# Kernel optimization log

Measured on AMD Instinct MI355X. Metric: run time of the kernel, lower is better.

The kernel has to match this reference:

```python
import jax, jax.numpy as jnp
import numpy as np
import math

DIMS = 2560
N_HEADS = 32
ROT_DIM = 32  # partial rotary (Phi-2)
BASE = 10000.0
B, L = 1, 2048


def apply_rope(x, rot_dim=ROT_DIM, base=BASE, offset=0):
    # x: [B, H, L, hd]; rotate first rot_dim features, pass rest through
    Lx = x.shape[2]
    D = rot_dim // 2
    pos = jnp.arange(offset, offset + Lx, dtype=jnp.float32)              # [L]
    freq = jnp.exp(-jnp.arange(D, dtype=jnp.float32) * (math.log(base) / D))  # [D]
    theta = pos[:, None] * freq[None, :]                                   # [L, D]
    cos, sin = jnp.cos(theta), jnp.sin(theta)
    x1 = x[..., :D]
    x2 = x[..., D:rot_dim]
    rx1 = x1 * cos - x2 * sin
    rx2 = x1 * sin + x2 * cos
    return jnp.concatenate([rx1, rx2, x[..., rot_dim:]], axis=-1)


def setup_inputs() -> dict:
    key = jax.random.key(0)
    k1, k2, k3, k4, k5 = jax.random.split(key, 5)
    x = jax.random.normal(k1, (B, L, DIMS), dtype=jnp.float32)
    Wqkv_w = jax.random.normal(k2, (3 * DIMS, DIMS), dtype=jnp.float32) * 0.02
    Wqkv_b = jax.random.normal(k3, (3 * DIMS,), dtype=jnp.float32) * 0.02
    out_w = jax.random.normal(k4, (DIMS, DIMS), dtype=jnp.float32) * 0.02
    out_b = jax.random.normal(k5, (DIMS,), dtype=jnp.float32) * 0.02
    # additive causal mask, broadcast over batch/heads
    mask = jnp.triu(jnp.full((L, L), -1e9, dtype=jnp.float32), k=1)[None, None]
    return {"x": x, "Wqkv_w": Wqkv_w, "Wqkv_b": Wqkv_b,
            "out_w": out_w, "out_b": out_b, "mask": mask}


def reference(x, Wqkv_w, Wqkv_b, out_w, out_b, mask):
    Bx, Lx, _ = x.shape
    hd = DIMS // N_HEADS  # 80
    qkv = x @ Wqkv_w.T + Wqkv_b                          # [B, L, 3*dims]
    q, k, v = jnp.split(qkv, 3, axis=-1)
    def to_heads(t):
        return t.reshape(Bx, Lx, N_HEADS, hd).transpose(0, 2, 1, 3)  # [B,H,L,hd]
    q, k, v = to_heads(q), to_heads(k), to_heads(v)
    q = apply_rope(q)
    k = apply_rope(k)
    scale = 1.0 / math.sqrt(hd)
    scores = scale * jnp.einsum('bhqd,bhkd->bhqk', q, k) + mask  # [B,H,L,L]
    probs = jax.nn.softmax(scores, axis=-1)
    out = jnp.einsum('bhqk,bhkd->bhqd', probs, v)
    out = out.transpose(0, 2, 1, 3).reshape(Bx, Lx, DIMS)
    return out @ out_w.T + out_b
```

## Files before the change

kernel.cpp:

```cpp
#include <hip/hip_runtime.h>
#include <cstdint>
#include <cmath>

typedef __attribute__((ext_vector_type(4))) float f32x4;
typedef __attribute__((ext_vector_type(8))) short s16x8;

#define LOG2E 1.4426950408889634f

__device__ __forceinline__ unsigned short f2bf(float f) {
    unsigned int u = __float_as_uint(f);
    u += 0x7FFFu + ((u >> 16) & 1u);
    return (unsigned short)(u >> 16);
}
__device__ __forceinline__ float bf2f(unsigned short s) {
    return __uint_as_float(((unsigned int)s) << 16);
}

__device__ __forceinline__ void async_copy16(const void* g, void* l) {
    __builtin_amdgcn_global_load_lds(
        (const __attribute__((address_space(1))) unsigned int*)(uintptr_t)g,
        (__attribute__((address_space(3))) unsigned int*)(uintptr_t)l,
        16, 0, 0);
}

__global__ __launch_bounds__(256) void cast_bf16_kernel(const float* __restrict__ in,
                                                        unsigned short* __restrict__ out,
                                                        int n4) {
    int i = blockIdx.x * 256 + threadIdx.x;
    if (i < n4) {
        float4 v = ((const float4*)in)[i];
        ushort4 o;
        o.x = f2bf(v.x); o.y = f2bf(v.y); o.z = f2bf(v.z); o.w = f2bf(v.w);
        ((ushort4*)out)[i] = o;
    }
}

template <bool BF16_OUT>
__global__ __launch_bounds__(256) void gemm_bt(const unsigned short* __restrict__ A,
                                               const unsigned short* __restrict__ B,
                                               const float* __restrict__ bias,
                                               void* __restrict__ Cout,
                                               int M, int N, int K) {
    __shared__ unsigned short As[128 * 32];
    __shared__ unsigned short Bs[128 * 32];
    const int tid  = threadIdx.x;
    const int lane = tid & 63;
    const int wv   = tid >> 6;
    const int m0 = blockIdx.y * 128;
    const int n0 = blockIdx.x * 128;
    const int w_row = (wv >> 1) * 64;
    const int w_col = (wv & 1) * 64;
    const int fr = lane & 15;
    const int fo = (lane >> 4) * 8;
    const int srow = lane >> 2;
    const int scol = (lane & 3) * 8;
    const int c0 = wv * 2;

    f32x4 acc[4][4];
    const f32x4 zf = {0.f, 0.f, 0.f, 0.f};
    for (int r = 0; r < 4; ++r)
        for (int c = 0; c < 4; ++c) acc[r][c] = zf;

    for (int k0 = 0; k0 < K; k0 += 32) {
        for (int c = c0; c < c0 + 2; ++c) {
            const unsigned short* gA = A + (size_t)(m0 + c * 16 + srow) * K + (k0 + scol);
            async_copy16(gA, &As[c * 512]);
            const unsigned short* gB = B + (size_t)(n0 + c * 16 + srow) * K + (k0 + scol);
            async_copy16(gB, &Bs[c * 512]);
        }
        __syncthreads();
        s16x8 af[4], bf[4];
        for (int r = 0; r < 4; ++r)
            af[r] = *(const s16x8*)&As[(w_row + r * 16 + fr) * 32 + fo];
        for (int c = 0; c < 4; ++c)
            bf[c] = *(const s16x8*)&Bs[(w_col + c * 16 + fr) * 32 + fo];
        for (int r = 0; r < 4; ++r)
            for (int c = 0; c < 4; ++c)
                acc[r][c] = __builtin_amdgcn_mfma_f32_16x16x32_bf16(af[r], bf[c], acc[r][c], 0, 0, 0);
        __syncthreads();
    }

    const int rb = (lane >> 4) * 4;
    for (int c = 0; c < 4; ++c) {
        int col = n0 + w_col + c * 16 + fr;
        float bv = bias[col];
        for (int r = 0; r < 4; ++r) {
            int row = m0 + w_row + r * 16 + rb;
            for (int q = 0; q < 4; ++q) {
                float v = acc[r][c][q] + bv;
                if constexpr (BF16_OUT)
                    ((unsigned short*)Cout)[(size_t)(row + q) * N + col] = f2bf(v);
                else
                    ((float*)Cout)[(size_t)(row + q) * N + col] = v;
            }
        }
    }
}

__global__ __launch_bounds__(256) void rope_kernel(unsigned short* __restrict__ qkv) {
    int g = blockIdx.x * 256 + threadIdx.x;
    int p = g >> 10;
    int i = g & 1023;
    int qk = i >> 9;
    int rem = i & 511;
    int hh = rem >> 4;
    int d = rem & 15;
    size_t base = (size_t)p * 7680 + qk * 2560 + hh * 80 + d;
    float x1 = bf2f(qkv[base]);
    float x2 = bf2f(qkv[base + 16]);
    float freq = expf(-(float)d * 0.57564627324851142f);
    float th = (float)p * freq;
    float s, c;
    sincosf(th, &s, &c);
    qkv[base]      = f2bf(x1 * c - x2 * s);
    qkv[base + 16] = f2bf(x1 * s + x2 * c);
}

__global__ __launch_bounds__(256) void pack_k_kernel(const unsigned short* __restrict__ qkv,
                                                     unsigned short* __restrict__ Kp) {
    int g = blockIdx.x * 256 + threadIdx.x;
    int c   = g % 12;
    int h   = (g / 12) & 31;
    int pos = g / 384;
    int d = c * 8;
    s16x8 v = {0, 0, 0, 0, 0, 0, 0, 0};
    if (d < 80)
        v = *(const s16x8*)(qkv + (size_t)pos * 7680 + 2560 + h * 80 + d);
    *(s16x8*)(Kp + ((size_t)h * 2048 + pos) * 96 + d) = v;
}

__global__ __launch_bounds__(256) void pack_v_kernel(const unsigned short* __restrict__ qkv,
                                                     unsigned short* __restrict__ Vp) {
    int h  = blockIdx.x & 31;
    int g64 = blockIdx.x >> 5;
    int k0 = g64 * 64;
    int tid = threadIdx.x;
    for (int ci = tid; ci < 320; ci += 256) {
        int d   = ci % 80;
        int kbl = ci / 80;
        unsigned short tmp[16];
        for (int j = 0; j < 16; ++j)
            tmp[j] = qkv[(size_t)(k0 + kbl * 16 + j) * 7680 + 5120 + h * 80 + d];
        unsigned short* dst = Vp + ((size_t)h * 128 + g64 * 4 + kbl) * 1280 + d * 16;
        *(s16x8*)dst       = *(const s16x8*)&tmp[0];
        *(s16x8*)(dst + 8) = *(const s16x8*)&tmp[8];
    }
}

__global__ __launch_bounds__(256) void flash3_kernel(const unsigned short* __restrict__ qkv,
                                                     const unsigned short* __restrict__ Kp,
                                                     const unsigned short* __restrict__ Vp,
                                                     unsigned short* __restrict__ attn) {
    __shared__ unsigned short Pt[4][640];
    __shared__ float parts[2][16][84];
    __shared__ float parts_l[2][16];
    const int tid  = threadIdx.x;
    const int lane = tid & 63;
    const int wv   = tid >> 6;
    const int h = blockIdx.x & 31;
    const int p = blockIdx.x >> 5;
    const int s    = (wv < 2) ? p : (127 - p);
    const int j    = wv & 1;
    const int slot = wv >> 1;
    const int fr = lane & 15;
    const int fg = lane >> 4;
    const float k1 = 0.11180339887498949f * LOG2E;
    const int sm16 = s * 16;

    const int n    = s + 1;
    const int half = (n + 1) >> 1;
    const int kstart = (j ? half : 0) * 16;
    const int kend   = (j ? n : half) * 16;

    s16x8 qf[3];
    {
        const unsigned short* qb = qkv + (size_t)(sm16 + fr) * 7680 + h * 80;
        const s16x8 zs = {0, 0, 0, 0, 0, 0, 0, 0};
        for (int sd = 0; sd < 3; ++sd) {
            int d = 32 * sd + fg * 8;
            qf[sd] = (d < 80) ? *(const s16x8*)(qb + d) : zs;
        }
    }

    f32x4 O[5];
    const f32x4 zf = {0.f, 0.f, 0.f, 0.f};
    for (int t = 0; t < 5; ++t) O[t] = zf;
    float rs[4] = {0.f, 0.f, 0.f, 0.f};

    const unsigned short* kptr = Kp + (size_t)h * 2048 * 96 + (size_t)(kstart + fr) * 96 + fg * 8;
    const unsigned short* vptr = Vp + (size_t)h * 128 * 1280 + (size_t)(kstart >> 4) * 1280
                                 + (fg >> 1) * 1280 + fr * 16 + (fg & 1) * 8;
    unsigned short* Pw = &Pt[wv][0];

    for (int k0 = kstart; k0 < kend; k0 += 32) {
        s16x8 kb[2][3];
        for (int g = 0; g < 2; ++g)
            for (int sd = 0; sd < 3; ++sd)
                kb[g][sd] = *(const s16x8*)(kptr + g * 1536 + sd * 32);
        s16x8 vb[5];
        for (int t = 0; t < 5; ++t)
            vb[t] = *(const s16x8*)(vptr + t * 256);

        f32x4 sa[2] = {zf, zf};
        for (int g = 0; g < 2; ++g)
            for (int sd = 0; sd < 3; ++sd)
                sa[g] = __builtin_amdgcn_mfma_f32_16x16x32_bf16(qf[sd], kb[g][sd], sa[g], 0, 0, 0);

        if (k0 + 32 > sm16 || k0 + 32 > kend) {
            for (int g = 0; g < 2; ++g)
                for (int r = 0; r < 4; ++r) {
                    int key  = k0 + g * 16 + fr;
                    int qrow = sm16 + fg * 4 + r;
                    if (key > qrow || key >= kend) sa[g][r] = -1e30f;
                }
        }

        float pr[2][4];
        for (int g = 0; g < 2; ++g)
            for (int r = 0; r < 4; ++r)
                pr[g][r] = __builtin_amdgcn_exp2f(sa[g][r] * k1);
        for (int r = 0; r < 4; ++r) rs[r] += pr[0][r] + pr[1][r];
        for (int g = 0; g < 2; ++g)
            for (int r = 0; r < 4; ++r)
                Pw[(fg * 4 + r) * 40 + g * 16 + fr] =
                    (unsigned short)(__float_as_uint(pr[g][r]) >> 16);

        s16x8 pa = *(const s16x8*)(Pw + fr * 40 + fg * 8);
        for (int t = 0; t < 5; ++t)
            O[t] = __builtin_amdgcn_mfma_f32_16x16x32_bf16(pa, vb[t], O[t], 0, 0, 0);

        kptr += 3072;
        vptr += 2560;
    }

    for (int r = 0; r < 4; ++r) {
        float v = rs[r];
        v += __shfl_xor(v, 1);
        v += __shfl_xor(v, 2);
        v += __shfl_xor(v, 4);
        v += __shfl_xor(v, 8);
        rs[r] = v;
    }

    if (j) {
        for (int t = 0; t < 5; ++t)
            for (int r = 0; r < 4; ++r)
                parts[slot][fg * 4 + r][t * 16 + fr] = O[t][r];
        if (fr == 0)
            for (int r = 0; r < 4; ++r) parts_l[slot][fg * 4 + r] = rs[r];
    }
    __syncthreads();
    if (!j) {
        for (int r = 0; r < 4; ++r) {
            float rl = 1.0f / (rs[r] + parts_l[slot][fg * 4 + r]);
            int row = sm16 + fg * 4 + r;
            for (int t = 0; t < 5; ++t) {
                float v = (O[t][r] + parts[slot][fg * 4 + r][t * 16 + fr]) * rl;
                attn[(size_t)row * 2560 + h * 80 + t * 16 + fr] = f2bf(v);
            }
        }
    }
}

extern "C" void kernel_launch(void* const* d_in, const int* in_sizes, int n_in,
                              void* d_out, int out_size, void* d_ws, size_t ws_size,
                              hipStream_t stream) {
    const float* x    = (const float*)d_in[0];
    const float* wqkv = (const float*)d_in[1];
    const float* bqkv = (const float*)d_in[2];
    const float* outw = (const float*)d_in[3];
    const float* outb = (const float*)d_in[4];

    unsigned short* xb    = (unsigned short*)d_ws;
    unsigned short* wqkvb = xb + (size_t)2048 * 2560;
    unsigned short* Kp    = wqkvb;
    unsigned short* Vp    = wqkvb + (size_t)32 * 2048 * 96;
    unsigned short* outwb = wqkvb + (size_t)7680 * 2560;
    unsigned short* qkvb  = outwb + (size_t)2560 * 2560;
    unsigned short* attnb = qkvb  + (size_t)2048 * 7680;
    float* out = (float*)d_out;

    cast_bf16_kernel<<<2048 * 2560 / 4 / 256, 256, 0, stream>>>(x, xb, 2048 * 2560 / 4);
    cast_bf16_kernel<<<7680 * 2560 / 4 / 256, 256, 0, stream>>>(wqkv, wqkvb, 7680 * 2560 / 4);
    cast_bf16_kernel<<<2560 * 2560 / 4 / 256, 256, 0, stream>>>(outw, outwb, 2560 * 2560 / 4);

    gemm_bt<true><<<dim3(7680 / 128, 2048 / 128), 256, 0, stream>>>(
        xb, wqkvb, bqkv, (void*)qkvb, 2048, 7680, 2560);

    rope_kernel<<<2048 * 1024 / 256, 256, 0, stream>>>(qkvb);

    pack_k_kernel<<<2048 * 384 / 256, 256, 0, stream>>>(qkvb, Kp);
    pack_v_kernel<<<32 * 32, 256, 0, stream>>>(qkvb, Vp);

    flash3_kernel<<<2048, 256, 0, stream>>>(qkvb, Kp, Vp, attnb);

    gemm_bt<false><<<dim3(2560 / 128, 2048 / 128), 256, 0, stream>>>(
        attnb, outwb, outb, (void*)out, 2048, 2560, 2560);
}
```

Baseline: 473.5 us.

## Swizzle GEMM LDS tiles, split-K output GEMM with atomics, fuse RoPE into K pack

The GEMM now XOR-swizzles the column offsets used for LDS writes and fragment reads, aiming to cut bank conflicts. The output projection is split along K into two z-slices that accumulate with float atomics into a zeroed output, which doubles the block count (the grid is only 320 tiles). RoPE is applied to K inside the packing kernel, and Q RoPE is vectorised to 8 elements per thread, which removes a separate pass over K. The cost is an extra memset, atomic traffic on the output, and a summation order that is no longer deterministic.

```diff
diff --git a/kernel.cpp b/kernel.cpp
--- a/kernel.cpp
+++ b/kernel.cpp
@@ -35,7 +35,7 @@
     }
 }
 
-template <bool BF16_OUT>
+template <bool BF16_OUT, bool ATOMIC>
 __global__ __launch_bounds__(256) void gemm_bt(const unsigned short* __restrict__ A,
                                                const unsigned short* __restrict__ B,
                                                const float* __restrict__ bias,
@@ -51,17 +51,24 @@
     const int w_row = (wv >> 1) * 64;
     const int w_col = (wv & 1) * 64;
     const int fr = lane & 15;
-    const int fo = (lane >> 4) * 8;
+    const int fg = lane >> 4;
     const int srow = lane >> 2;
-    const int scol = (lane & 3) * 8;
+    const int scol = (((lane & 3) ^ ((lane >> 3) & 3)) * 8);
+    const int rofs = ((fg ^ ((fr >> 1) & 3)) * 8);
     const int c0 = wv * 2;
+
+    int kstart = 0, kend = K;
+    if (ATOMIC) {
+        kstart = blockIdx.z * (K >> 1);
+        kend   = kstart + (K >> 1);
+    }
 
     f32x4 acc[4][4];
     const f32x4 zf = {0.f, 0.f, 0.f, 0.f};
     for (int r = 0; r < 4; ++r)
         for (int c = 0; c < 4; ++c) acc[r][c] = zf;
 
-    for (int k0 = 0; k0 < K; k0 += 32) {
+    for (int k0 = kstart; k0 < kend; k0 += 32) {
         for (int c = c0; c < c0 + 2; ++c) {
             const unsigned short* gA = A + (size_t)(m0 + c * 16 + srow) * K + (k0 + scol);
             async_copy16(gA, &As[c * 512]);
@@ -71,9 +78,9 @@
         __syncthreads();
         s16x8 af[4], bf[4];
         for (int r = 0; r < 4; ++r)
-            af[r] = *(const s16x8*)&As[(w_row + r * 16 + fr) * 32 + fo];
+            af[r] = *(const s16x8*)&As[(w_row + r * 16 + fr) * 32 + rofs];
         for (int c = 0; c < 4; ++c)
-            bf[c] = *(const s16x8*)&Bs[(w_col + c * 16 + fr) * 32 + fo];
+            bf[c] = *(const s16x8*)&Bs[(w_col + c * 16 + fr) * 32 + rofs];
         for (int r = 0; r < 4; ++r)
             for (int c = 0; c < 4; ++c)
                 acc[r][c] = __builtin_amdgcn_mfma_f32_16x16x32_bf16(af[r], bf[c], acc[r][c], 0, 0, 0);
@@ -81,52 +88,84 @@
     }
 
     const int rb = (lane >> 4) * 4;
+    const bool addb = !ATOMIC || blockIdx.z == 0;
     for (int c = 0; c < 4; ++c) {
         int col = n0 + w_col + c * 16 + fr;
-        float bv = bias[col];
+        float bv = addb ? bias[col] : 0.f;
         for (int r = 0; r < 4; ++r) {
             int row = m0 + w_row + r * 16 + rb;
             for (int q = 0; q < 4; ++q) {
                 float v = acc[r][c][q] + bv;
-                if constexpr (BF16_OUT)
+                if constexpr (ATOMIC) {
+                    unsafeAtomicAdd(&((float*)Cout)[(size_t)(row + q) * N + col], v);
+                } else if constexpr (BF16_OUT) {
                     ((unsigned short*)Cout)[(size_t)(row + q) * N + col] = f2bf(v);
-                else
+                } else {
                     ((float*)Cout)[(size_t)(row + q) * N + col] = v;
+                }
             }
         }
     }
 }
 
-__global__ __launch_bounds__(256) void rope_kernel(unsigned short* __restrict__ qkv) {
+__global__ __launch_bounds__(256) void rope_q_kernel(unsigned short* __restrict__ qkv) {
     int g = blockIdx.x * 256 + threadIdx.x;
-    int p = g >> 10;
-    int i = g & 1023;
-    int qk = i >> 9;
-    int rem = i & 511;
-    int hh = rem >> 4;
-    int d = rem & 15;
-    size_t base = (size_t)p * 7680 + qk * 2560 + hh * 80 + d;
-    float x1 = bf2f(qkv[base]);
-    float x2 = bf2f(qkv[base + 16]);
-    float freq = expf(-(float)d * 0.57564627324851142f);
-    float th = (float)p * freq;
-    float s, c;
-    sincosf(th, &s, &c);
-    qkv[base]      = f2bf(x1 * c - x2 * s);
-    qkv[base + 16] = f2bf(x1 * s + x2 * c);
-}
-
-__global__ __launch_bounds__(256) void pack_k_kernel(const unsigned short* __restrict__ qkv,
-                                                     unsigned short* __restrict__ Kp) {
+    int c = g & 1;
+    int h = (g >> 1) & 31;
+    int p = g >> 6;
+    size_t base = (size_t)p * 7680 + h * 80 + c * 8;
+    s16x8 x1v = *(const s16x8*)(qkv + base);
+    s16x8 x2v = *(const s16x8*)(qkv + base + 16);
+    s16x8 o1, o2;
+    for (int j = 0; j < 8; ++j) {
+        int dp = c * 8 + j;
+        float freq = expf(-(float)dp * 0.57564627324851142f);
+        float sn, cs;
+        sincosf((float)p * freq, &sn, &cs);
+        float x1 = bf2f((unsigned short)x1v[j]);
+        float x2 = bf2f((unsigned short)x2v[j]);
+        o1[j] = (short)f2bf(x1 * cs - x2 * sn);
+        o2[j] = (short)f2bf(x1 * sn + x2 * cs);
+    }
+    *(s16x8*)(qkv + base)      = o1;
+    *(s16x8*)(qkv + base + 16) = o2;
+}
+
+__global__ __launch_bounds__(256) void rope_pack_k_kernel(const unsigned short* __restrict__ qkv,
+                                                          unsigned short* __restrict__ Kp) {
     int g = blockIdx.x * 256 + threadIdx.x;
     int c   = g % 12;
     int h   = (g / 12) & 31;
     int pos = g / 384;
-    int d = c * 8;
+    int d0 = c * 8;
+    const unsigned short* kb = qkv + (size_t)pos * 7680 + 2560 + h * 80;
     s16x8 v = {0, 0, 0, 0, 0, 0, 0, 0};
-    if (d < 80)
-        v = *(const s16x8*)(qkv + (size_t)pos * 7680 + 2560 + h * 80 + d);
-    *(s16x8*)(Kp + ((size_t)h * 2048 + pos) * 96 + d) = v;
+    if (c >= 4) {
+        if (d0 < 80) v = *(const s16x8*)(kb + d0);
+    } else if (c < 2) {
+        s16x8 x1v = *(const s16x8*)(kb + d0);
+        s16x8 x2v = *(const s16x8*)(kb + d0 + 16);
+        for (int j = 0; j < 8; ++j) {
+            int dp = d0 + j;
+            float freq = expf(-(float)dp * 0.57564627324851142f);
+            float sn, cs;
+            sincosf((float)pos * freq, &sn, &cs);
+            v[j] = (short)f2bf(bf2f((unsigned short)x1v[j]) * cs -
+                               bf2f((unsigned short)x2v[j]) * sn);
+        }
+    } else {
+        s16x8 x1v = *(const s16x8*)(kb + d0 - 16);
+        s16x8 x2v = *(const s16x8*)(kb + d0);
+        for (int j = 0; j < 8; ++j) {
+            int dp = d0 - 16 + j;
+            float freq = expf(-(float)dp * 0.57564627324851142f);
+            float sn, cs;
+            sincosf((float)pos * freq, &sn, &cs);
+            v[j] = (short)f2bf(bf2f((unsigned short)x1v[j]) * sn +
+                               bf2f((unsigned short)x2v[j]) * cs);
+        }
+    }
+    *(s16x8*)(Kp + ((size_t)h * 2048 + pos) * 96 + d0) = v;
 }
 
 __global__ __launch_bounds__(256) void pack_v_kernel(const unsigned short* __restrict__ qkv,
@@ -284,16 +323,16 @@
     cast_bf16_kernel<<<7680 * 2560 / 4 / 256, 256, 0, stream>>>(wqkv, wqkvb, 7680 * 2560 / 4);
     cast_bf16_kernel<<<2560 * 2560 / 4 / 256, 256, 0, stream>>>(outw, outwb, 2560 * 2560 / 4);
 
-    gemm_bt<true><<<dim3(7680 / 128, 2048 / 128), 256, 0, stream>>>(
+    gemm_bt<true, false><<<dim3(7680 / 128, 2048 / 128), 256, 0, stream>>>(
         xb, wqkvb, bqkv, (void*)qkvb, 2048, 7680, 2560);
 
-    rope_kernel<<<2048 * 1024 / 256, 256, 0, stream>>>(qkvb);
-
-    pack_k_kernel<<<2048 * 384 / 256, 256, 0, stream>>>(qkvb, Kp);
+    rope_q_kernel<<<2048 * 64 / 256, 256, 0, stream>>>(qkvb);
+    rope_pack_k_kernel<<<2048 * 384 / 256, 256, 0, stream>>>(qkvb, Kp);
     pack_v_kernel<<<32 * 32, 256, 0, stream>>>(qkvb, Vp);
 
     flash3_kernel<<<2048, 256, 0, stream>>>(qkvb, Kp, Vp, attnb);
 
-    gemm_bt<false><<<dim3(2560 / 128, 2048 / 128), 256, 0, stream>>>(
+    hipMemsetAsync(d_out, 0, (size_t)2048 * 2560 * 4, stream);
+    gemm_bt<false, true><<<dim3(2560 / 128, 2048 / 128, 2), 256, 0, stream>>>(
         attnb, outwb, outb, (void*)out, 2048, 2560, 2560);
 }
```

Measured after the change: 492.2 us. 1.04x slower.
